# Kernel optimization log

Hardware: AMD Instinct MI355X
Metric: run time of the kernel (lower is better)

## Reference

```python
import jax, jax.numpy as jnp
import numpy as np

NIN = 4096
NOUT = 4096
LN_EPS = 1e-5  # torch.nn.LayerNorm default


def setup_inputs() -> dict:
    key = jax.random.key(0)
    ks = jax.random.split(key, 8)
    x = jax.random.normal(ks[0], (1, NIN), dtype=jnp.float32)
    hid = jax.random.normal(ks[1], (1, NOUT), dtype=jnp.float32)
    hebb = jnp.zeros((NOUT, NOUT), dtype=jnp.float32) + 1e-6  # initialZeroHebb
    # parameters
    w_in = 0.01 * jax.random.normal(ks[2], (NOUT, NIN), dtype=jnp.float32)  # inp_lin weight (no bias)
    w = 0.01 * jnp.eye(NOUT, NOUT, dtype=jnp.float32)                        # Plastic.w
    alpha = 0.01 * jax.random.normal(ks[3], (NOUT, NOUT), dtype=jnp.float32)
    b = 0.01 * jax.random.normal(ks[4], (NOUT,), dtype=jnp.float32)
    lamda = 0.01 * jnp.ones((1,), dtype=jnp.float32)
    pred_eta = 0.01 * jax.random.normal(ks[5], (NOUT, NOUT), dtype=jnp.float32)
    pred_eta_b = 0.01 * jax.random.normal(ks[6], (NOUT,), dtype=jnp.float32)
    ln_gamma = jnp.ones((NOUT,), dtype=jnp.float32)
    ln_beta = jnp.zeros((NOUT,), dtype=jnp.float32)
    return {"x": x, "hid": hid, "hebb": hebb, "w_in": w_in, "w": w,
            "alpha": alpha, "b": b, "lamda": lamda, "pred_eta": pred_eta,
            "pred_eta_b": pred_eta_b, "ln_gamma": ln_gamma, "ln_beta": ln_beta}


def reference(x, hid, hebb, w_in, w, alpha, b, lamda, pred_eta, pred_eta_b, ln_gamma, ln_beta):
    # Cell.forward (nonlin = ReLU for both wx and the post-LN output)
    wx = jax.nn.relu(x @ w_in.T)                       # [1, nout]
    wh = hid @ (w + alpha * hebb) + b                  # Plastic.forward, [1, nout]
    s = wx + wh
    mu = jnp.mean(s, axis=-1, keepdims=True)
    var = jnp.mean((s - mu) ** 2, axis=-1, keepdims=True)
    ln = ln_gamma * (s - mu) * jax.lax.rsqrt(var + LN_EPS) + ln_beta
    wy = jax.nn.relu(ln)                               # new hidden state, [1, nout]
    # Plastic.update_hebb(x=hid, y=wh, hebb)
    eta_hat = jax.nn.sigmoid(wh @ pred_eta + pred_eta_b)           # [1, nout]
    outer = hid[0, :, None] * wh[0, None, :]                        # [nout, nout]
    hebb_new = (1.0 - lamda) * hebb + eta_hat.T * outer             # row i scaled by eta_hat[0, i]
    return wy, hebb_new
```

## Files before the change

kernel.cpp:

```cpp
#include <hip/hip_runtime.h>
#include <hip/hip_bf16.h>
#include <math.h>

#define N 4096

__inline__ __device__ float waveReduceSum(float v) {
    #pragma unroll
    for (int o = 32; o > 0; o >>= 1) v += __shfl_down(v, o);
    return v;
}

__global__ __launch_bounds__(256) void k_wx(const float* __restrict__ x,
                                            const float* __restrict__ w_in,
                                            float* __restrict__ wx_out) {
    int j = blockIdx.x;
    const float4* row = reinterpret_cast<const float4*>(w_in + (size_t)j * N);
    const float4* xv  = reinterpret_cast<const float4*>(x);
    float sum = 0.f;
    #pragma unroll 4
    for (int k = threadIdx.x; k < N / 4; k += 256) {
        float4 a = row[k], c = xv[k];
        sum += a.x * c.x + a.y * c.y + a.z * c.z + a.w * c.w;
    }
    sum = waveReduceSum(sum);
    __shared__ float wsum[4];
    int wid = threadIdx.x >> 6, lane = threadIdx.x & 63;
    if (lane == 0) wsum[wid] = sum;
    __syncthreads();
    if (threadIdx.x == 0) {
        float t = wsum[0] + wsum[1] + wsum[2] + wsum[3];
        wx_out[j] = fmaxf(t, 0.f);
    }
}

__global__ __launch_bounds__(256) void k_wh_part(const float* __restrict__ hid,
                                                 const float* __restrict__ w,
                                                 const float* __restrict__ alpha,
                                                 const float* __restrict__ hebb,
                                                 float* __restrict__ part) {
    int j  = blockIdx.x * 256 + threadIdx.x;
    int i0 = blockIdx.y * 64;
    float sum = 0.f;
    #pragma unroll 4
    for (int i = i0; i < i0 + 64; ++i) {
        size_t off = (size_t)i * N + j;
        sum = fmaf(hid[i], fmaf(alpha[off], hebb[off], w[off]), sum);
    }
    part[(size_t)blockIdx.y * N + j] = sum;
}

__global__ __launch_bounds__(1024) void k_ln(const float* __restrict__ part,
                                             const float* __restrict__ b,
                                             const float* __restrict__ wx,
                                             const float* __restrict__ gamma,
                                             const float* __restrict__ beta,
                                             float* __restrict__ wh_out,
                                             float* __restrict__ wy_out) {
    __shared__ float red[16];
    __shared__ float bc[2];
    int tid = threadIdx.x;
    int wid = tid >> 6, lane = tid & 63;
    float sv[4];
    float lsum = 0.f;
    #pragma unroll
    for (int q = 0; q < 4; ++q) {
        int j = q * 1024 + tid;
        float acc = b[j];
        for (int c = 0; c < 64; ++c) acc += part[(size_t)c * N + j];
        wh_out[j] = acc;
        float s = acc + wx[j];
        sv[q] = s;
        lsum += s;
    }
    float wv = waveReduceSum(lsum);
    if (lane == 0) red[wid] = wv;
    __syncthreads();
    if (tid < 64) {
        float t = (tid < 16) ? red[tid] : 0.f;
        t = waveReduceSum(t);
        if (tid == 0) bc[0] = t * (1.f / N);
    }
    __syncthreads();
    float mean = bc[0];
    __syncthreads();
    float lsq = 0.f;
    #pragma unroll
    for (int q = 0; q < 4; ++q) { float d = sv[q] - mean; lsq += d * d; }
    wv = waveReduceSum(lsq);
    if (lane == 0) red[wid] = wv;
    __syncthreads();
    if (tid < 64) {
        float t = (tid < 16) ? red[tid] : 0.f;
        t = waveReduceSum(t);
        if (tid == 0) bc[1] = t * (1.f / N);
    }
    __syncthreads();
    float rstd = rsqrtf(bc[1] + 1e-5f);
    #pragma unroll
    for (int q = 0; q < 4; ++q) {
        int j = q * 1024 + tid;
        float ln = fmaf(gamma[j] * (sv[q] - mean), rstd, beta[j]);
        wy_out[j] = fmaxf(ln, 0.f);
    }
}

__global__ __launch_bounds__(256) void k_eta_part(const float* __restrict__ wh,
                                                  const float* __restrict__ pe,
                                                  float* __restrict__ part) {
    int j  = blockIdx.x * 256 + threadIdx.x;
    int i0 = blockIdx.y * 64;
    float sum = 0.f;
    #pragma unroll 4
    for (int i = i0; i < i0 + 64; ++i) {
        sum = fmaf(wh[i], pe[(size_t)i * N + j], sum);
    }
    part[(size_t)blockIdx.y * N + j] = sum;
}

__global__ __launch_bounds__(256) void k_eta_fin(const float* __restrict__ part,
                                                 const float* __restrict__ pb,
                                                 float* __restrict__ eta) {
    int j = blockIdx.x * 256 + threadIdx.x;
    float s = pb[j];
    for (int c = 0; c < 64; ++c) s += part[(size_t)c * N + j];
    eta[j] = 1.f / (1.f + expf(-s));
}

__global__ __launch_bounds__(256) void k_hebb(const float* __restrict__ hebb,
                                              const float* __restrict__ eta,
                                              const float* __restrict__ hid,
                                              const float* __restrict__ wh,
                                              const float* __restrict__ lamda,
                                              float* __restrict__ out) {
    int i  = blockIdx.y;
    int j0 = blockIdx.x * 1024 + threadIdx.x * 4;
    float decay = 1.f - lamda[0];
    float coef  = eta[i] * hid[i];
    const float4 h  = *reinterpret_cast<const float4*>(hebb + (size_t)i * N + j0);
    const float4 w4 = *reinterpret_cast<const float4*>(wh + j0);
    float4 r;
    r.x = fmaf(decay, h.x, coef * w4.x);
    r.y = fmaf(decay, h.y, coef * w4.y);
    r.z = fmaf(decay, h.z, coef * w4.z);
    r.w = fmaf(decay, h.w, coef * w4.w);
    *reinterpret_cast<float4*>(out + (size_t)i * N + j0) = r;
}

extern "C" void kernel_launch(void* const* d_in, const int* in_sizes, int n_in,
                              void* d_out, int out_size, void* d_ws, size_t ws_size,
                              hipStream_t stream) {
    const float* x         = (const float*)d_in[0];
    const float* hid       = (const float*)d_in[1];
    const float* hebb      = (const float*)d_in[2];
    const float* w_in      = (const float*)d_in[3];
    const float* w         = (const float*)d_in[4];
    const float* alpha     = (const float*)d_in[5];
    const float* b         = (const float*)d_in[6];
    const float* lamda     = (const float*)d_in[7];
    const float* pred_eta  = (const float*)d_in[8];
    const float* pred_eta_b= (const float*)d_in[9];
    const float* ln_gamma  = (const float*)d_in[10];
    const float* ln_beta   = (const float*)d_in[11];

    float* wy       = (float*)d_out;
    float* hebb_out = (float*)d_out + N;

    float* ws   = (float*)d_ws;
    float* part = ws;
    float* wx   = ws + 64 * N;
    float* wh   = ws + 64 * N + N;
    float* eta  = ws + 64 * N + 2 * N;

    k_wx      <<<N, 256, 0, stream>>>(x, w_in, wx);
    k_wh_part <<<dim3(16, 64), 256, 0, stream>>>(hid, w, alpha, hebb, part);
    k_ln      <<<1, 1024, 0, stream>>>(part, b, wx, ln_gamma, ln_beta, wh, wy);
    k_eta_part<<<dim3(16, 64), 256, 0, stream>>>(wh, pred_eta, part);
    k_eta_fin <<<16, 256, 0, stream>>>(part, pred_eta_b, eta);
    k_hebb    <<<dim3(4, N), 256, 0, stream>>>(hebb, eta, hid, wh, lamda, hebb_out);
}
```

Before: 106.6 us.

## Fuse wx/wh matvecs into one launch and fuse eta with hebb update

Merges the wx GEMV and the plastic wh partial sums into a single grid, using more independent blocks and nontemporal vector loads. A two-stage reduction now feeds the layernorm kernel. The eta projection is fused with the hebb update so each block computes its 16 eta values and then writes those hebb rows with nontemporal stores. This cuts launch count and keeps more loads in flight over the large matrices, at the cost of more complex indexing and a fallback path that depends on workspace size.

```diff
diff --git a/kernel.cpp b/kernel.cpp
--- a/kernel.cpp
+++ b/kernel.cpp
@@ -3,6 +3,9 @@
 #include <math.h>
 
 #define N 4096
+#define NGRP 16
+
+typedef float f32x4 __attribute__((ext_vector_type(4)));
 
 __inline__ __device__ float waveReduceSum(float v) {
     #pragma unroll
@@ -10,48 +13,91 @@
     return v;
 }
 
-__global__ __launch_bounds__(256) void k_wx(const float* __restrict__ x,
-                                            const float* __restrict__ w_in,
-                                            float* __restrict__ wx_out) {
-    int j = blockIdx.x;
-    const float4* row = reinterpret_cast<const float4*>(w_in + (size_t)j * N);
-    const float4* xv  = reinterpret_cast<const float4*>(x);
-    float sum = 0.f;
-    #pragma unroll 4
-    for (int k = threadIdx.x; k < N / 4; k += 256) {
-        float4 a = row[k], c = xv[k];
-        sum += a.x * c.x + a.y * c.y + a.z * c.z + a.w * c.w;
-    }
-    sum = waveReduceSum(sum);
-    __shared__ float wsum[4];
-    int wid = threadIdx.x >> 6, lane = threadIdx.x & 63;
-    if (lane == 0) wsum[wid] = sum;
-    __syncthreads();
-    if (threadIdx.x == 0) {
-        float t = wsum[0] + wsum[1] + wsum[2] + wsum[3];
-        wx_out[j] = fmaxf(t, 0.f);
-    }
-}
-
-__global__ __launch_bounds__(256) void k_wh_part(const float* __restrict__ hid,
-                                                 const float* __restrict__ w,
-                                                 const float* __restrict__ alpha,
-                                                 const float* __restrict__ hebb,
-                                                 float* __restrict__ part) {
-    int j  = blockIdx.x * 256 + threadIdx.x;
-    int i0 = blockIdx.y * 64;
-    float sum = 0.f;
-    #pragma unroll 4
-    for (int i = i0; i < i0 + 64; ++i) {
-        size_t off = (size_t)i * N + j;
-        sum = fmaf(hid[i], fmaf(alpha[off], hebb[off], w[off]), sum);
-    }
-    part[(size_t)blockIdx.y * N + j] = sum;
-}
-
-__global__ __launch_bounds__(1024) void k_ln(const float* __restrict__ part,
+#define LD4(p, o) (*reinterpret_cast<const float4*>((p) + (o)))
+
+__inline__ __device__ f32x4 ntld4(const float* p) {
+    return __builtin_nontemporal_load(reinterpret_cast<const f32x4*>(p));
+}
+
+template<int ITERS>
+__global__ __launch_bounds__(256) void k_phase1(const float* __restrict__ x,
+                                                const float* __restrict__ w_in,
+                                                const float* __restrict__ hid,
+                                                const float* __restrict__ w,
+                                                const float* __restrict__ alpha,
+                                                const float* __restrict__ hebb,
+                                                float* __restrict__ part,
+                                                float* __restrict__ wx_out,
+                                                int G) {
+    int t = threadIdx.x;
+    if ((int)blockIdx.x < G) {
+        int b = blockIdx.x;
+        int p = b >> 2;
+        int P = G >> 2;
+        int j0 = (((b & 3) << 8) | t) * 4;
+        size_t step = (size_t)G * 1024;
+        size_t off = (size_t)(((b << 8) | t)) * 4;
+
+        f32x4 wv[ITERS], av[ITERS], bv[ITERS];
+        float hv[ITERS];
+        #pragma unroll
+        for (int k = 0; k < ITERS; ++k) {
+            size_t o = off + (size_t)k * step;
+            wv[k] = ntld4(w + o);
+            av[k] = ntld4(alpha + o);
+            bv[k] = *reinterpret_cast<const f32x4*>(hebb + o);
+        }
+        #pragma unroll
+        for (int k = 0; k < ITERS; ++k) hv[k] = hid[k * P + p];
+
+        f32x4 acc = {0.f, 0.f, 0.f, 0.f};
+        #pragma unroll
+        for (int k = 0; k < ITERS; ++k) {
+            float h = hv[k];
+            acc.x = fmaf(h, fmaf(av[k].x, bv[k].x, wv[k].x), acc.x);
+            acc.y = fmaf(h, fmaf(av[k].y, bv[k].y, wv[k].y), acc.y);
+            acc.z = fmaf(h, fmaf(av[k].z, bv[k].z, wv[k].z), acc.z);
+            acc.w = fmaf(h, fmaf(av[k].w, bv[k].w, wv[k].w), acc.w);
+        }
+        *reinterpret_cast<f32x4*>(part + (size_t)p * N + j0) = acc;
+    } else {
+        int j = blockIdx.x - G;
+        const float4* row = reinterpret_cast<const float4*>(w_in + (size_t)j * N);
+        const float4* xv  = reinterpret_cast<const float4*>(x);
+        float sum = 0.f;
+        #pragma unroll
+        for (int k = t; k < N / 4; k += 256) {
+            float4 a = row[k], c = xv[k];
+            sum += a.x * c.x + a.y * c.y + a.z * c.z + a.w * c.w;
+        }
+        sum = waveReduceSum(sum);
+        __shared__ float wsum[4];
+        int wid = t >> 6, lane = t & 63;
+        if (lane == 0) wsum[wid] = sum;
+        __syncthreads();
+        if (t == 0)
+            wx_out[j] = fmaxf(wsum[0] + wsum[1] + wsum[2] + wsum[3], 0.f);
+    }
+}
+
+__global__ __launch_bounds__(256) void k_red(const float* __restrict__ part,
+                                             float* __restrict__ part2,
+                                             int cpg) {
+    int g  = blockIdx.y;
+    int j0 = (blockIdx.x * 256 + threadIdx.x) * 4;
+    const float4* p4 = reinterpret_cast<const float4*>(part);
+    float4 s = make_float4(0.f, 0.f, 0.f, 0.f);
+    #pragma unroll 8
+    for (int c = 0; c < cpg; ++c) {
+        float4 v = p4[((size_t)(g * cpg + c) * N + j0) >> 2];
+        s.x += v.x; s.y += v.y; s.z += v.z; s.w += v.w;
+    }
+    *reinterpret_cast<float4*>(part2 + (size_t)g * N + j0) = s;
+}
+
+__global__ __launch_bounds__(1024) void k_ln(const float* __restrict__ part2,
+                                             const float* __restrict__ wx,
                                              const float* __restrict__ b,
-                                             const float* __restrict__ wx,
                                              const float* __restrict__ gamma,
                                              const float* __restrict__ beta,
                                              float* __restrict__ wh_out,
@@ -66,7 +112,8 @@
     for (int q = 0; q < 4; ++q) {
         int j = q * 1024 + tid;
         float acc = b[j];
-        for (int c = 0; c < 64; ++c) acc += part[(size_t)c * N + j];
+        #pragma unroll
+        for (int g = 0; g < NGRP; ++g) acc += part2[(size_t)g * N + j];
         wh_out[j] = acc;
         float s = acc + wx[j];
         sv[q] = s;
@@ -104,46 +151,56 @@
     }
 }
 
-__global__ __launch_bounds__(256) void k_eta_part(const float* __restrict__ wh,
-                                                  const float* __restrict__ pe,
-                                                  float* __restrict__ part) {
-    int j  = blockIdx.x * 256 + threadIdx.x;
-    int i0 = blockIdx.y * 64;
-    float sum = 0.f;
+__global__ __launch_bounds__(1024) void k_eta_hebb(const float* __restrict__ pe,
+                                                   const float* __restrict__ pb,
+                                                   const float* __restrict__ wh,
+                                                   const float* __restrict__ hid,
+                                                   const float* __restrict__ lamda,
+                                                   const float* __restrict__ hebb,
+                                                   float* __restrict__ out) {
+    __shared__ float sm[64][17];
+    __shared__ float coef_s[16];
+    int t  = threadIdx.x;
+    int i0 = blockIdx.x * 16;
+    int cl = t & 15;
+    int g  = t >> 4;
+    int c  = i0 + cl;
+
+    float acc = 0.f;
+    const float* perow = pe + (size_t)(g * 64) * N + c;
+    const float* whp   = wh + g * 64;
+    #pragma unroll 8
+    for (int k = 0; k < 64; ++k)
+        acc = fmaf(whp[k], perow[(size_t)k * N], acc);
+    sm[g][cl] = acc;
+    __syncthreads();
+    #pragma unroll
+    for (int off = 32; off >= 1; off >>= 1) {
+        if (g < off) sm[g][cl] += sm[g + off][cl];
+        __syncthreads();
+    }
+    if (t < 16) {
+        int i = i0 + t;
+        float eta = 1.f / (1.f + expf(-(sm[0][t] + pb[i])));
+        coef_s[t] = eta * hid[i];
+    }
+    __syncthreads();
+
+    float decay = 1.f - lamda[0];
+    int j = (t & 1023) * 4;
+    float4 w4 = LD4(wh, j);
+    size_t base = (size_t)i0 * N + j;
     #pragma unroll 4
-    for (int i = i0; i < i0 + 64; ++i) {
-        sum = fmaf(wh[i], pe[(size_t)i * N + j], sum);
-    }
-    part[(size_t)blockIdx.y * N + j] = sum;
-}
-
-__global__ __launch_bounds__(256) void k_eta_fin(const float* __restrict__ part,
-                                                 const float* __restrict__ pb,
-                                                 float* __restrict__ eta) {
-    int j = blockIdx.x * 256 + threadIdx.x;
-    float s = pb[j];
-    for (int c = 0; c < 64; ++c) s += part[(size_t)c * N + j];
-    eta[j] = 1.f / (1.f + expf(-s));
-}
-
-__global__ __launch_bounds__(256) void k_hebb(const float* __restrict__ hebb,
-                                              const float* __restrict__ eta,
-                                              const float* __restrict__ hid,
-                                              const float* __restrict__ wh,
-                                              const float* __restrict__ lamda,
-                                              float* __restrict__ out) {
-    int i  = blockIdx.y;
-    int j0 = blockIdx.x * 1024 + threadIdx.x * 4;
-    float decay = 1.f - lamda[0];
-    float coef  = eta[i] * hid[i];
-    const float4 h  = *reinterpret_cast<const float4*>(hebb + (size_t)i * N + j0);
-    const float4 w4 = *reinterpret_cast<const float4*>(wh + j0);
-    float4 r;
-    r.x = fmaf(decay, h.x, coef * w4.x);
-    r.y = fmaf(decay, h.y, coef * w4.y);
-    r.z = fmaf(decay, h.z, coef * w4.z);
-    r.w = fmaf(decay, h.w, coef * w4.w);
-    *reinterpret_cast<float4*>(out + (size_t)i * N + j0) = r;
+    for (int r = 0; r < 16; ++r) {
+        float coef = coef_s[r];
+        float4 h = LD4(hebb, base + (size_t)r * N);
+        f32x4 o;
+        o.x = fmaf(decay, h.x, coef * w4.x);
+        o.y = fmaf(decay, h.y, coef * w4.y);
+        o.z = fmaf(decay, h.z, coef * w4.z);
+        o.w = fmaf(decay, h.w, coef * w4.w);
+        __builtin_nontemporal_store(o, reinterpret_cast<f32x4*>(out + base + (size_t)r * N));
+    }
 }
 
 extern "C" void kernel_launch(void* const* d_in, const int* in_sizes, int n_in,
@@ -165,16 +222,23 @@
     float* wy       = (float*)d_out;
     float* hebb_out = (float*)d_out + N;
 
-    float* ws   = (float*)d_ws;
-    float* part = ws;
-    float* wx   = ws + 64 * N;
-    float* wh   = ws + 64 * N + N;
-    float* eta  = ws + 64 * N + 2 * N;
-
-    k_wx      <<<N, 256, 0, stream>>>(x, w_in, wx);
-    k_wh_part <<<dim3(16, 64), 256, 0, stream>>>(hid, w, alpha, hebb, part);
-    k_ln      <<<1, 1024, 0, stream>>>(part, b, wx, ln_gamma, ln_beta, wh, wy);
-    k_eta_part<<<dim3(16, 64), 256, 0, stream>>>(wh, pred_eta, part);
-    k_eta_fin <<<16, 256, 0, stream>>>(part, pred_eta_b, eta);
-    k_hebb    <<<dim3(4, N), 256, 0, stream>>>(hebb, eta, hid, wh, lamda, hebb_out);
-}
+    int G = 2048;
+    if ((ws_size / 4) < ((size_t)(G / 4) * N + (NGRP + 2) * (size_t)N)) G = 512;
+    int P = G / 4;
+    int cpg = P / NGRP;
+
+    float* ws    = (float*)d_ws;
+    float* part  = ws;
+    float* part2 = part + (size_t)P * N;
+    float* wx    = part2 + (size_t)NGRP * N;
+    float* wh    = wx + N;
+
+    if (G == 2048) {
+        k_phase1<8><<<G + N, 256, 0, stream>>>(x, w_in, hid, w, alpha, hebb, part, wx, G);
+    } else {
+        k_phase1<32><<<G + N, 256, 0, stream>>>(x, w_in, hid, w, alpha, hebb, part, wx, G);
+    }
+    k_red     <<<dim3(4, NGRP), 256, 0, stream>>>(part, part2, cpg);
+    k_ln      <<<1, 1024, 0, stream>>>(part2, wx, b, ln_gamma, ln_beta, wh, wy);
+    k_eta_hebb<<<256, 1024, 0, stream>>>(pred_eta, pred_eta_b, wh, hid, lamda, hebb, hebb_out);
+}
```

New measurement: 98.03 us. -8.1%, faster.
